# Kernel tuning notes

Hardware: AMD Instinct MI355X
Metric: run time of the kernel (lower is better)

## Reference

```python
import jax, jax.numpy as jnp
import numpy as np

D_MODEL, D_STATE, HEAD_DIM, EXPAND, K, N_GROUPS = 1024, 128, 64, 2, 4, 1
D_INNER = EXPAND * D_MODEL            # 2048
N_HEADS = D_INNER // HEAD_DIM         # 32
D_PROJ = 2 * D_INNER + 2 * N_GROUPS * D_STATE + N_HEADS  # 4384
EPS = 1e-6


def setup_inputs() -> dict:
    key = jax.random.key(0)
    ks = jax.random.split(key, 8)
    B, L = 2, 2048
    x = jax.random.normal(ks[0], (B, L, D_MODEL), dtype=jnp.float32)
    norm_w = jnp.ones((D_MODEL,), jnp.float32)
    in_proj_w = jax.random.normal(ks[1], (D_PROJ, D_MODEL), jnp.float32) * (D_MODEL ** -0.5)
    conv_w = jax.random.normal(ks[2], (D_INNER, 1, K), jnp.float32) * (K ** -0.5)
    conv_b = jnp.zeros((D_INNER,), jnp.float32)
    A_log = jnp.log(jax.random.uniform(ks[3], (N_HEADS,)) * 15.0 + 1.0)
    D = jnp.ones((N_HEADS,), jnp.float32)
    dt_bias = jnp.log(jax.random.uniform(ks[4], (N_HEADS,)) * 0.099 + 0.001)
    out_proj_w = jax.random.normal(ks[5], (D_MODEL, D_INNER), jnp.float32) * (D_INNER ** -0.5)
    return {"x": x, "norm_w": norm_w, "in_proj_w": in_proj_w, "conv_w": conv_w,
            "conv_b": conv_b, "A_log": A_log, "D": D, "dt_bias": dt_bias,
            "out_proj_w": out_proj_w}


def _silu(v):
    return v * jax.nn.sigmoid(v)


def reference(x, norm_w, in_proj_w, conv_w, conv_b, A_log, D, dt_bias, out_proj_w):
    Bsz, L, _ = x.shape
    residual = x
    # RMSNorm (pre-norm)
    xn = x * jax.lax.rsqrt(jnp.mean(x * x, axis=-1, keepdims=True) + EPS) * norm_w
    proj = xn @ in_proj_w.T                                     # (B, L, D_PROJ)
    # split fused projection -> (z, x_ssm, B, C, dt_raw)
    i = 0
    z = proj[..., i:i + D_INNER]; i += D_INNER
    x_ssm = proj[..., i:i + D_INNER]; i += D_INNER
    bc = N_GROUPS * D_STATE
    Bm = proj[..., i:i + bc].reshape(Bsz, L, N_GROUPS, D_STATE); i += bc
    Cm = proj[..., i:i + bc].reshape(Bsz, L, N_GROUPS, D_STATE); i += bc
    dt_raw = proj[..., i:i + N_HEADS]
    # causal depthwise conv1d (torch pad=K-1 then slice [:L] == left-pad K-1)
    xc = jnp.transpose(x_ssm, (0, 2, 1))                        # (B, D_INNER, L)
    xc = jax.lax.conv_general_dilated(
        xc, conv_w, window_strides=(1,), padding=[(K - 1, 0)],
        dimension_numbers=("NCH", "OIH", "NCH"), feature_group_count=D_INNER)
    xc = xc + conv_b[None, :, None]
    x_conv = _silu(jnp.transpose(xc, (0, 2, 1)))                # (B, L, D_INNER)
    # discretisation
    dt = jax.nn.softplus(dt_raw + dt_bias)                      # (B, L, H)
    dA = jnp.exp(-jnp.exp(A_log)[None, None, :] * dt)           # (B, L, H)
    x_heads = x_conv.reshape(Bsz, L, N_HEADS, HEAD_DIM)
    dt_x = dt[..., None] * x_heads                              # (B, L, H, P)
    group_idx = jnp.arange(N_HEADS) // (N_HEADS // N_GROUPS)
    Bg = Bm[:, :, group_idx, :]                                 # (B, L, H, N)
    Cg = Cm[:, :, group_idx, :]
    # sequential selective scan over time via lax.scan (fp32 state)
    def step(h, inp):
        dA_t, dtx_t, B_t, C_t = inp                             # (B,H),(B,H,P),(B,H,N),(B,H,N)
        h = h * dA_t[..., None, None] + dtx_t[..., None] * B_t[:, :, None, :]
        y_t = jnp.einsum("bhpn,bhn->bhp", h, C_t)
        return h, y_t
    h0 = jnp.zeros((Bsz, N_HEADS, HEAD_DIM, D_STATE), jnp.float32)
    xs = (jnp.moveaxis(dA, 1, 0).astype(jnp.float32),
          jnp.moveaxis(dt_x, 1, 0).astype(jnp.float32),
          jnp.moveaxis(Bg, 1, 0).astype(jnp.float32),
          jnp.moveaxis(Cg, 1, 0).astype(jnp.float32))
    _, y = jax.lax.scan(step, h0, xs)                           # y: (L, B, H, P)
    y = jnp.moveaxis(y, 0, 1).astype(x.dtype)                   # (B, L, H, P)
    y = y + D[None, None, :, None] * x_heads
    y = y.reshape(Bsz, L, D_INNER) * _silu(z)                   # gated output
    return residual + y @ out_proj_w.T
```

## Files before the change

kernel.cpp:

```cpp
#include <hip/hip_runtime.h>
#include <math.h>

#define B_SZ     2
#define L_SEQ    2048
#define DM       1024
#define DP       4384
#define PS       4480
#define DI       2048
#define NH       32
#define HD       64
#define DS       128
#define M_ROWS   (B_SZ * L_SEQ)
#define QCH      64
#define NC       (L_SEQ / QCH)

typedef __bf16 bf16x8 __attribute__((ext_vector_type(8)));
typedef __bf16 bf16x4 __attribute__((ext_vector_type(4)));
typedef float  f32x4  __attribute__((ext_vector_type(4)));

__global__ __launch_bounds__(256) void k_prep(const float* __restrict__ Wp,
                                              __bf16* __restrict__ Wpb,
                                              const float* __restrict__ x,
                                              const float* __restrict__ w,
                                              __bf16* __restrict__ xn) {
    int tid = threadIdx.x;
    if (blockIdx.x < 4384) {
        int i = blockIdx.x * 256 + tid;
        float4 v = ((const float4*)Wp)[i];
        bf16x4 o = { (__bf16)v.x, (__bf16)v.y, (__bf16)v.z, (__bf16)v.w };
        ((bf16x4*)Wpb)[i] = o;
        return;
    }
    int row = blockIdx.x - 4384;
    const float4* x4 = (const float4*)(x + (long)row * DM);
    float4 v = x4[tid];
    float ss = v.x * v.x + v.y * v.y + v.z * v.z + v.w * v.w;
    #pragma unroll
    for (int off = 32; off > 0; off >>= 1) ss += __shfl_xor(ss, off, 64);
    __shared__ float sred[4];
    if ((tid & 63) == 0) sred[tid >> 6] = ss;
    __syncthreads();
    float tot = sred[0] + sred[1] + sred[2] + sred[3];
    float scale = rsqrtf(tot * (1.0f / (float)DM) + 1e-6f);
    const float4* w4 = (const float4*)w;
    float4 wv = w4[tid];
    bf16x4 o = { (__bf16)(v.x * scale * wv.x), (__bf16)(v.y * scale * wv.y),
                 (__bf16)(v.z * scale * wv.z), (__bf16)(v.w * scale * wv.w) };
    ((bf16x4*)(xn + (long)row * DM))[tid] = o;
}

__global__ __launch_bounds__(256) void k_gemm_bf(const __bf16* __restrict__ A,
                                                 const __bf16* __restrict__ W,
                                                 const float* __restrict__ resid,
                                                 float* __restrict__ Cf,
                                                 __bf16* __restrict__ Cb,
                                                 float* __restrict__ Dt,
                                                 int Nw, int K, int ldc) {
    __shared__ __align__(16) __bf16 As[128 * 64];
    __shared__ __align__(16) __bf16 Bs[128 * 64];
    int t = threadIdx.x;
    int bm = blockIdx.y * 128, bn = blockIdx.x * 128;

    int r0 = t >> 2;
    int lc = t & 3;
    int r1 = r0 + 64;
    const __bf16* Ag0 = A + (long)(bm + r0) * K + lc * 8;
    const __bf16* Ag1 = A + (long)(bm + r1) * K + lc * 8;
    int br0 = bn + r0; if (br0 >= Nw) br0 = Nw - 1;
    int br1 = bn + r1; if (br1 >= Nw) br1 = Nw - 1;
    const __bf16* Wg0 = W + (long)br0 * K + lc * 8;
    const __bf16* Wg1 = W + (long)br1 * K + lc * 8;

    int sw0  = r0 * 64 + (((lc    ) ^ (r0 & 7)) << 3);
    int sw0b = r0 * 64 + (((lc + 4) ^ (r0 & 7)) << 3);
    int sw1  = r1 * 64 + (((lc    ) ^ (r1 & 7)) << 3);
    int sw1b = r1 * 64 + (((lc + 4) ^ (r1 & 7)) << 3);

    int lane = t & 63, w = t >> 6;
    int wm = (w & 1) * 64, wn = (w >> 1) * 64;
    int ln = lane & 15;
    int q  = lane >> 4;

    f32x4 acc[4][4] = {};

    for (int k0 = 0; k0 < K; k0 += 64) {
        bf16x8 a0  = *(const bf16x8*)(Ag0 + k0);
        bf16x8 a0b = *(const bf16x8*)(Ag0 + k0 + 32);
        bf16x8 a1  = *(const bf16x8*)(Ag1 + k0);
        bf16x8 a1b = *(const bf16x8*)(Ag1 + k0 + 32);
        bf16x8 b0  = *(const bf16x8*)(Wg0 + k0);
        bf16x8 b0b = *(const bf16x8*)(Wg0 + k0 + 32);
        bf16x8 b1  = *(const bf16x8*)(Wg1 + k0);
        bf16x8 b1b = *(const bf16x8*)(Wg1 + k0 + 32);
        __syncthreads();
        *(bf16x8*)(As + sw0)  = a0;  *(bf16x8*)(As + sw0b) = a0b;
        *(bf16x8*)(As + sw1)  = a1;  *(bf16x8*)(As + sw1b) = a1b;
        *(bf16x8*)(Bs + sw0)  = b0;  *(bf16x8*)(Bs + sw0b) = b0b;
        *(bf16x8*)(Bs + sw1)  = b1;  *(bf16x8*)(Bs + sw1b) = b1b;
        __syncthreads();

        #pragma unroll
        for (int h = 0; h < 2; h++) {
            int ch = (4 * h + q);
            int koff = ((ch ^ (ln & 7)) << 3);
            bf16x8 af[4], bfr[4];
            #pragma unroll
            for (int i = 0; i < 4; i++)
                af[i]  = *(const bf16x8*)(As + (wm + ln + i * 16) * 64 + koff);
            #pragma unroll
            for (int j = 0; j < 4; j++)
                bfr[j] = *(const bf16x8*)(Bs + (wn + ln + j * 16) * 64 + koff);
            #pragma unroll
            for (int i = 0; i < 4; i++)
                #pragma unroll
                for (int j = 0; j < 4; j++)
                    acc[i][j] = __builtin_amdgcn_mfma_f32_16x16x32_bf16(
                                    af[i], bfr[j], acc[i][j], 0, 0, 0);
        }
    }

    int colbase = bn + wn + ln;
    #pragma unroll
    for (int i = 0; i < 4; i++) {
        #pragma unroll
        for (int r = 0; r < 4; r++) {
            int m = bm + wm + i * 16 + (lane >> 4) * 4 + r;
            long off = (long)m * ldc + colbase;
            #pragma unroll
            for (int j = 0; j < 4; j++) {
                float v = acc[i][j][r];
                if (Cb != nullptr) {
                    Cb[off + j * 16] = (__bf16)v;
                    if (Dt != nullptr) {
                        int col = colbase + j * 16;
                        if (col >= 4352 && col < 4384)
                            Dt[(long)m * 32 + (col - 4352)] = v;
                    }
                } else {
                    if (resid != nullptr) v += resid[off + j * 16];
                    Cf[off + j * 16] = v;
                }
            }
        }
    }
}

__global__ __launch_bounds__(256) void k_chunk(const __bf16* __restrict__ projb,
                                               const float* __restrict__ dtraw,
                                               const float* __restrict__ cw,
                                               const float* __restrict__ cb,
                                               const float* __restrict__ A_log,
                                               const float* __restrict__ dt_bias,
                                               const float* __restrict__ Dv,
                                               float* __restrict__ clog,
                                               __bf16* __restrict__ yssm,
                                               float* __restrict__ Sloc) {
    int blk = blockIdx.x;
    int c  = blk & 31;
    int hh = (blk >> 5) & 31;
    int b  = blk >> 10;
    int tid = threadIdx.x;
    long rowbase = (long)b * L_SEQ + c * QCH;

    __shared__ __align__(16) __bf16 sB[64 * 136];
    __shared__ __align__(16) __bf16 sU[128 * 72];
    __shared__ __align__(16) __bf16 sXT[64 * 72];
    __shared__ __align__(16) __bf16 sXCM[67 * 72];
    __shared__ __align__(16) __bf16 sXCo[64 * 72];
    __shared__ float sCW[256];
    __shared__ float sCB[64];
    __shared__ float sclog[64];
    __shared__ float sdt[64];
    __shared__ float sw[64];

    #pragma unroll
    for (int j = 0; j < 4; j++) {
        int off = j * 256 + tid;
        int t  = off >> 4;
        int n8 = (off & 15) * 8;
        const __bf16* pr = projb + (rowbase + t) * (long)PS;
        *(bf16x8*)&sB[t * 136 + n8] = *(const bf16x8*)(pr + 4096 + n8);
        *(bf16x8*)&sU[t * 136 + n8] = *(const bf16x8*)(pr + 4224 + n8);
    }
    #pragma unroll
    for (int j = 0; j < 3; j++) {
        int off = j * 256 + tid;
        if (off < 536) {
            int ss = off >> 3;
            int p8 = (off & 7) * 8;
            bf16x8 xv;
            #pragma unroll
            for (int k = 0; k < 8; k++) xv[k] = (__bf16)0.0f;
            if (c > 0 || ss >= 3)
                xv = *(const bf16x8*)(projb + (rowbase + ss - 3) * (long)PS + DI + hh * HD + p8);
            *(bf16x8*)&sXCM[ss * 72 + p8] = xv;
        }
    }
    sCW[tid] = cw[hh * 256 + tid];
    if (tid < 64) sCB[tid] = cb[hh * 64 + tid];

    if (tid < 64) {
        float xr = dtraw[(rowbase + tid) * 32 + hh] + dt_bias[hh];
        float dt = (xr > 20.0f) ? xr : log1pf(expf(xr));
        float la = -expf(A_log[hh]);
        float v = la * dt;
        #pragma unroll
        for (int off = 1; off < 64; off <<= 1) {
            float u = __shfl_up(v, off, 64);
            if (tid >= off) v += u;
        }
        sdt[tid] = dt;
        sclog[tid] = v;
        clog[(rowbase + tid) * NH + hh] = v;
    }
    __syncthreads();

    {
        int p8 = (tid & 7) * 8;
        float wreg[8][4], breg[8];
        #pragma unroll
        for (int e = 0; e < 8; e++) {
            breg[e] = sCB[p8 + e];
            #pragma unroll
            for (int j = 0; j < 4; j++) wreg[e][j] = sCW[(p8 + e) * 4 + j];
        }
        #pragma unroll
        for (int i = 0; i < 2; i++) {
            int s = i * 32 + (tid >> 3);
            bf16x8 r0 = *(const bf16x8*)&sXCM[(s + 0) * 72 + p8];
            bf16x8 r1 = *(const bf16x8*)&sXCM[(s + 1) * 72 + p8];
            bf16x8 r2 = *(const bf16x8*)&sXCM[(s + 2) * 72 + p8];
            bf16x8 r3 = *(const bf16x8*)&sXCM[(s + 3) * 72 + p8];
            float dts = sdt[s];
            bf16x8 oc;
            #pragma unroll
            for (int e = 0; e < 8; e++) {
                float acc = breg[e];
                acc = fmaf(wreg[e][0], (float)r0[e], acc);
                acc = fmaf(wreg[e][1], (float)r1[e], acc);
                acc = fmaf(wreg[e][2], (float)r2[e], acc);
                acc = fmaf(wreg[e][3], (float)r3[e], acc);
                float xc = acc / (1.0f + expf(-acc));
                oc[e] = (__bf16)xc;
                sXT[(p8 + e) * 72 + s] = (__bf16)(dts * xc);
            }
            *(bf16x8*)&sXCo[s * 72 + p8] = oc;
        }
    }
    if (tid < 64) sw[tid] = expf(sclog[63] - sclog[tid]);
    __syncthreads();

    int lane = tid & 63, w = tid >> 6;
    int ln = lane & 15;
    int quad = lane >> 4;
    int kc = quad * 8;

    bf16x8 caf[4];
    #pragma unroll
    for (int k0 = 0; k0 < 4; k0++)
        caf[k0] = *(const bf16x8*)&sU[(16 * w + ln) * 136 + kc + k0 * 32];
    f32x4 g[4] = {};
    #pragma unroll
    for (int j = 0; j < 4; j++)
        #pragma unroll
        for (int k0 = 0; k0 < 4; k0++) {
            bf16x8 bf_ = *(const bf16x8*)&sB[(16 * j + ln) * 136 + kc + k0 * 32];
            g[j] = __builtin_amdgcn_mfma_f32_16x16x32_bf16(caf[k0], bf_, g[j], 0, 0, 0);
        }

    {
        int trow = 16 * w + quad * 4;
        #pragma unroll
        for (int r = 0; r < 4; r++) {
            int t = trow + r;
            float ct = sclog[t];
            #pragma unroll
            for (int j = 0; j < 4; j++) {
                int s = 16 * j + ln;
                float v = (s <= t) ? g[j][r] * expf(ct - sclog[s]) : 0.0f;
                sXCM[t * 72 + s] = (__bf16)v;
            }
        }
    }
    __syncthreads();

    #pragma unroll
    for (int j = 0; j < 4; j++) {
        int s  = tid & 63;
        int n8 = (j * 4 + (tid >> 6)) * 8;
        bf16x8 v = *(const bf16x8*)&sB[s * 136 + n8];
        #pragma unroll
        for (int k = 0; k < 8; k++) sU[(n8 + k) * 72 + s] = v[k];
    }

    {
        float Dh = Dv[hh];
        bf16x8 maf[2];
        #pragma unroll
        for (int k0 = 0; k0 < 2; k0++)
            maf[k0] = *(const bf16x8*)&sXCM[(16 * w + ln) * 72 + kc + k0 * 32];
        f32x4 y[4] = {};
        #pragma unroll
        for (int j = 0; j < 4; j++)
            #pragma unroll
            for (int k0 = 0; k0 < 2; k0++) {
                bf16x8 xf = *(const bf16x8*)&sXT[(16 * j + ln) * 72 + kc + k0 * 32];
                y[j] = __builtin_amdgcn_mfma_f32_16x16x32_bf16(maf[k0], xf, y[j], 0, 0, 0);
            }
        #pragma unroll
        for (int j = 0; j < 4; j++)
            #pragma unroll
            for (int r = 0; r < 4; r++) {
                int t = 16 * w + quad * 4 + r;
                int p = 16 * j + ln;
                float v = y[j][r] + Dh * (float)sXCo[t * 72 + p];
                yssm[(rowbase + t) * DI + hh * HD + p] = (__bf16)v;
            }
    }
    __syncthreads();

    {
        bf16x8 xaf[2];
        #pragma unroll
        for (int k0 = 0; k0 < 2; k0++) {
            bf16x8 raw = *(const bf16x8*)&sXT[(16 * w + ln) * 72 + kc + k0 * 32];
            bf16x8 sc;
            #pragma unroll
            for (int jj = 0; jj < 8; jj++) {
                int s = kc + k0 * 32 + jj;
                sc[jj] = (__bf16)((float)raw[jj] * sw[s]);
            }
            xaf[k0] = sc;
        }
        f32x4 sacc[8] = {};
        #pragma unroll
        for (int j = 0; j < 8; j++)
            #pragma unroll
            for (int k0 = 0; k0 < 2; k0++) {
                bf16x8 btf = *(const bf16x8*)&sU[(16 * j + ln) * 72 + kc + k0 * 32];
                sacc[j] = __builtin_amdgcn_mfma_f32_16x16x32_bf16(xaf[k0], btf, sacc[j], 0, 0, 0);
            }
        long sbase = ((long)(b * NH + hh) * NC + c) * (HD * DS);
        #pragma unroll
        for (int j = 0; j < 8; j++)
            #pragma unroll
            for (int r = 0; r < 4; r++) {
                int p = 16 * w + quad * 4 + r;
                int n = 16 * j + ln;
                Sloc[sbase + p * DS + n] = sacc[j][r];
            }
    }
}

__global__ __launch_bounds__(256) void k_carry_f2b(float* __restrict__ Sloc,
                                                   const float* __restrict__ clog,
                                                   const float* __restrict__ Wo,
                                                   __bf16* __restrict__ Wob) {
    int bid = blockIdx.x;
    int tid = threadIdx.x;
    if (bid >= 2048) {
        int i = (bid - 2048) * 256 + tid;
        float4 v = ((const float4*)Wo)[i];
        bf16x4 o = { (__bf16)v.x, (__bf16)v.y, (__bf16)v.z, (__bf16)v.w };
        ((bf16x4*)Wob)[i] = o;
        return;
    }
    int idx = bid * 256 + tid;
    int n  = idx & 127;
    int p  = (idx >> 7) & 63;
    int hh = (idx >> 13) & 31;
    int b  = idx >> 18;
    long base = ((long)(b * NH + hh) * NC) * (HD * DS) + p * DS + n;
    float T = 0.0f;
    for (int c = 0; c < NC; c++) {
        float lam = expf(clog[((long)b * L_SEQ + c * QCH + QCH - 1) * NH + hh]);
        long a = base + (long)c * (HD * DS);
        float S = Sloc[a];
        Sloc[a] = T;
        T = fmaf(T, lam, S);
    }
}

__global__ __launch_bounds__(256, 2) void k_fix(const __bf16* __restrict__ projb,
                                                const float* __restrict__ Sloc,
                                                const float* __restrict__ clog,
                                                const __bf16* __restrict__ yb,
                                                __bf16* __restrict__ yg) {
    int blk = blockIdx.x;
    int c  = blk & 31;
    int hh = (blk >> 5) & 31;
    int b  = blk >> 10;

    __shared__ __align__(16) __bf16 sC[64 * 136];
    __shared__ __align__(16) __bf16 sH[64 * 136];
    __shared__ float sP[64];

    int tid = threadIdx.x;
    long hbase = ((long)(b * NH + hh) * NC + c) * (HD * DS);
    long rowbase = (long)b * L_SEQ + c * QCH;

    #pragma unroll
    for (int j = 0; j < 4; j++) {
        int off = j * 256 + tid;
        int t  = off >> 4;
        int n8 = (off & 15) * 8;
        *(bf16x8*)&sC[t * 136 + n8] =
            *(const bf16x8*)(projb + (rowbase + t) * (long)PS + 4224 + n8);
    }
    #pragma unroll
    for (int j = 0; j < 8; j++) {
        int off = j * 256 + tid;
        int p  = off >> 5;
        int n4 = (off & 31) * 4;
        float4 hv = *(const float4*)&Sloc[hbase + (long)off * 4];
        bf16x4 hb = {(__bf16)hv.x, (__bf16)hv.y, (__bf16)hv.z, (__bf16)hv.w};
        *(bf16x4*)&sH[p * 136 + n4] = hb;
    }
    if (tid < 64) sP[tid] = expf(clog[(rowbase + tid) * NH + hh]);
    __syncthreads();

    int lane = tid & 63, w = tid >> 6;
    int ln = lane & 15;
    int quad = lane >> 4;
    int kc = quad * 8;

    bf16x8 caf[4];
    #pragma unroll
    for (int k0 = 0; k0 < 4; k0++)
        caf[k0] = *(const bf16x8*)&sC[(16 * w + ln) * 136 + kc + k0 * 32];
    f32x4 acc4[4] = {};
    #pragma unroll
    for (int j = 0; j < 4; j++)
        #pragma unroll
        for (int k0 = 0; k0 < 4; k0++) {
            bf16x8 hf = *(const bf16x8*)&sH[(16 * j + ln) * 136 + kc + k0 * 32];
            acc4[j] = __builtin_amdgcn_mfma_f32_16x16x32_bf16(caf[k0], hf, acc4[j], 0, 0, 0);
        }

    #pragma unroll
    for (int j = 0; j < 4; j++)
        #pragma unroll
        for (int r = 0; r < 4; r++) {
            int t = 16 * w + quad * 4 + r;
            int p = 16 * j + ln;
            long row = rowbase + t;
            long yoff = row * DI + hh * HD + p;
            float pm = sP[t];
            float z = (float)projb[row * (long)PS + hh * HD + p];
            float o = ((float)yb[yoff] + pm * acc4[j][r]) * (z / (1.0f + expf(-z)));
            yg[yoff] = (__bf16)o;
        }
}

extern "C" void kernel_launch(void* const* d_in, const int* in_sizes, int n_in,
                              void* d_out, int out_size, void* d_ws, size_t ws_size,
                              hipStream_t stream) {
    const float* x       = (const float*)d_in[0];
    const float* norm_w  = (const float*)d_in[1];
    const float* Wp      = (const float*)d_in[2];
    const float* cw      = (const float*)d_in[3];
    const float* cb      = (const float*)d_in[4];
    const float* A_log   = (const float*)d_in[5];
    const float* Dv      = (const float*)d_in[6];
    const float* dt_bias = (const float*)d_in[7];
    const float* Wo      = (const float*)d_in[8];
    float* out = (float*)d_out;

    float* ws     = (float*)d_ws;
    __bf16* projb = (__bf16*)ws;
    float* dtraw  = ws    + 9175040;
    float* clog   = dtraw + 131072;
    float* ybh    = clog  + 131072;
    float* ybf    = ybh   + 4194304;
    float* wob_s  = ybf   + 4194304;
    float* U      = wob_s + 1048576;

    __bf16* xnb  = (__bf16*)U;
    __bf16* Wpb  = (__bf16*)(U + 2097152);
    float*  Sloc = U;
    __bf16* Wob  = (__bf16*)wob_s;
    __bf16* ybb  = (__bf16*)ybf;
    __bf16* yb   = (__bf16*)ybh;

    k_prep<<<4384 + M_ROWS, 256, 0, stream>>>(Wp, Wpb, x, norm_w, xnb);
    {
        dim3 g(PS / 128, M_ROWS / 128);
        k_gemm_bf<<<g, 256, 0, stream>>>(xnb, Wpb, nullptr, nullptr, projb,
                                         dtraw, DP, DM, PS);
    }

    k_chunk<<<B_SZ * NH * NC, 256, 0, stream>>>(projb, dtraw, cw, cb, A_log,
                                                dt_bias, Dv, clog, yb, Sloc);
    k_carry_f2b<<<4096, 256, 0, stream>>>(Sloc, clog, Wo, Wob);
    k_fix<<<B_SZ * NH * NC, 256, 0, stream>>>(projb, Sloc, clog, yb, ybb);

    {
        dim3 g(DM / 128, M_ROWS / 128);
        k_gemm_bf<<<g, 256, 0, stream>>>(ybb, Wob, x, out, nullptr, nullptr,
                                         DM, DI, DM);
    }
}
```

Measured before the change: 307.9 us.

## Load GEMM tiles directly into LDS via global_load_lds and remap workgroups

Replaces register-staged global loads plus LDS stores in the bf16 GEMM with direct global-to-LDS 16-byte loads. Each wave writes contiguous 512-element chunks, with the XOR swizzle folded into the per-lane global column index so the existing swizzled read pattern still holds. It also remaps workgroup IDs in groups of 8 to change which tiles run together, aiming at better cache locality. The direct LDS path drops VGPR traffic and ds_write instructions. The risk is relying on implicit waitcnt before the barrier for correctness, and there is still no double buffering.

```diff
diff --git a/kernel.cpp b/kernel.cpp
--- a/kernel.cpp
+++ b/kernel.cpp
@@ -18,6 +18,13 @@
 typedef __bf16 bf16x4 __attribute__((ext_vector_type(4)));
 typedef float  f32x4  __attribute__((ext_vector_type(4)));
 
+__device__ __forceinline__ void gload16(const void* g, void* l) {
+    __builtin_amdgcn_global_load_lds(
+        (const __attribute__((address_space(1))) unsigned int*)g,
+        (__attribute__((address_space(3))) unsigned int*)l,
+        16, 0, 0);
+}
+
 __global__ __launch_bounds__(256) void k_prep(const float* __restrict__ Wp,
                                               __bf16* __restrict__ Wpb,
                                               const float* __restrict__ x,
@@ -59,24 +66,28 @@
     __shared__ __align__(16) __bf16 As[128 * 64];
     __shared__ __align__(16) __bf16 Bs[128 * 64];
     int t = threadIdx.x;
-    int bm = blockIdx.y * 128, bn = blockIdx.x * 128;
-
-    int r0 = t >> 2;
-    int lc = t & 3;
-    int r1 = r0 + 64;
-    const __bf16* Ag0 = A + (long)(bm + r0) * K + lc * 8;
-    const __bf16* Ag1 = A + (long)(bm + r1) * K + lc * 8;
-    int br0 = bn + r0; if (br0 >= Nw) br0 = Nw - 1;
-    int br1 = bn + r1; if (br1 >= Nw) br1 = Nw - 1;
-    const __bf16* Wg0 = W + (long)br0 * K + lc * 8;
-    const __bf16* Wg1 = W + (long)br1 * K + lc * 8;
-
-    int sw0  = r0 * 64 + (((lc    ) ^ (r0 & 7)) << 3);
-    int sw0b = r0 * 64 + (((lc + 4) ^ (r0 & 7)) << 3);
-    int sw1  = r1 * 64 + (((lc    ) ^ (r1 & 7)) << 3);
-    int sw1b = r1 * 64 + (((lc + 4) ^ (r1 & 7)) << 3);
+
+    int gx = gridDim.x;
+    int nwg = gx * gridDim.y;
+    int orig = blockIdx.y * gx + blockIdx.x;
+    int wgid = (nwg & 7) ? orig : ((orig & 7) * (nwg >> 3) + (orig >> 3));
+    int bx = wgid % gx, by = wgid / gx;
+    int bm = by * 128, bn = bx * 128;
 
     int lane = t & 63, w = t >> 6;
+
+    int rl = lane >> 3;
+    int lc = (lane & 7) ^ rl;
+    int rbase = w * 32 + rl;
+    const __bf16* Agp[4];
+    const __bf16* Wgp[4];
+    #pragma unroll
+    for (int i = 0; i < 4; i++) {
+        Agp[i] = A + (long)(bm + rbase + i * 8) * K + lc * 8;
+        int rb = bn + rbase + i * 8; if (rb >= Nw) rb = Nw - 1;
+        Wgp[i] = W + (long)rb * K + lc * 8;
+    }
+
     int wm = (w & 1) * 64, wn = (w >> 1) * 64;
     int ln = lane & 15;
     int q  = lane >> 4;
@@ -84,19 +95,12 @@
     f32x4 acc[4][4] = {};
 
     for (int k0 = 0; k0 < K; k0 += 64) {
-        bf16x8 a0  = *(const bf16x8*)(Ag0 + k0);
-        bf16x8 a0b = *(const bf16x8*)(Ag0 + k0 + 32);
-        bf16x8 a1  = *(const bf16x8*)(Ag1 + k0);
-        bf16x8 a1b = *(const bf16x8*)(Ag1 + k0 + 32);
-        bf16x8 b0  = *(const bf16x8*)(Wg0 + k0);
-        bf16x8 b0b = *(const bf16x8*)(Wg0 + k0 + 32);
-        bf16x8 b1  = *(const bf16x8*)(Wg1 + k0);
-        bf16x8 b1b = *(const bf16x8*)(Wg1 + k0 + 32);
         __syncthreads();
-        *(bf16x8*)(As + sw0)  = a0;  *(bf16x8*)(As + sw0b) = a0b;
-        *(bf16x8*)(As + sw1)  = a1;  *(bf16x8*)(As + sw1b) = a1b;
-        *(bf16x8*)(Bs + sw0)  = b0;  *(bf16x8*)(Bs + sw0b) = b0b;
-        *(bf16x8*)(Bs + sw1)  = b1;  *(bf16x8*)(Bs + sw1b) = b1b;
+        #pragma unroll
+        for (int i = 0; i < 4; i++) {
+            gload16(Agp[i] + k0, As + (w * 4 + i) * 512);
+            gload16(Wgp[i] + k0, Bs + (w * 4 + i) * 512);
+        }
         __syncthreads();
 
         #pragma unroll
```

After: 305.1 us. About the same (-0.9%).
